# Kernel tuning notes

Hardware: AMD Instinct MI355X
Metric: run time of the kernel (lower is better)

The kernel has to match this reference:

```python
import jax, jax.numpy as jnp
import numpy as np

NUM_FEATURES = 256
NUM_PIDS = 5532
CQ_SIZE = 5000
N_NONID = 256
N = 2048
OIM_SCALAR = 30.0
MOMENTUM = 0.5


def _unit_rows(key, shape):
    v = jax.random.normal(key, shape, dtype=jnp.float32)
    return v / jnp.linalg.norm(v, axis=-1, keepdims=True)


def setup_inputs() -> dict:
    key = jax.random.key(0)
    ks = jax.random.split(key, 8)
    inputs = _unit_rows(ks[0], (N, NUM_FEATURES))
    targets = jax.random.randint(ks[1], (N,), 0, NUM_PIDS + 100, dtype=jnp.int32)
    belong_to_first_half = jax.random.randint(ks[2], (N,), 0, 2) > 0
    non_id_feat = _unit_rows(ks[3], (N_NONID, NUM_FEATURES))
    lut = _unit_rows(ks[4], (NUM_PIDS, NUM_FEATURES))
    cq = _unit_rows(ks[5], (CQ_SIZE, NUM_FEATURES))
    first_pos_sample = _unit_rows(ks[6], (NUM_PIDS, NUM_FEATURES))
    second_pos_sample = _unit_rows(ks[7], (NUM_PIDS, NUM_FEATURES))
    return {
        "inputs": inputs,
        "non_id_feat": non_id_feat,
        "lut": lut,
        "cq": cq,
        "first_pos_sample": first_pos_sample,
        "second_pos_sample": second_pos_sample,
        "targets": targets,
        "belong_to_first_half": belong_to_first_half,
        "header": 0,
    }


def reference(inputs, non_id_feat, lut, cq, first_pos_sample, second_pos_sample,
              targets, belong_to_first_half, header):
    # OIM forward: similarities against labeled LUT and [circular queue; non-id feats]
    out_labeled = inputs @ lut.T                                  # [N, num_pids]
    out_unlabeled = inputs @ jnp.concatenate([cq, non_id_feat], 0).T  # [N, cq+nonid]
    projected = jnp.concatenate([out_labeled, out_unlabeled], axis=1)
    return projected * OIM_SCALAR
```

## Files before the change

### kernel.cpp

```cpp
#include <hip/hip_runtime.h>
#include <hip/hip_bf16.h>
#include <stdint.h>
#include <stddef.h>

#define NUM_FEATURES 256
#define NUM_PIDS 5532
#define CQ_SIZE 5000
#define N_NONID 256
#define N_ROWS 2048
#define N_COLS (NUM_PIDS + CQ_SIZE + N_NONID)
#define OIM_SCALAR 30.0f


#define BM 128
#define BN 128
#define BK 64
#define KITERS (NUM_FEATURES / BK)

#define NT_PER_XCD 11
#define N_TILES 85
#define M_TILES 16
#define GRID_BLOCKS (8 * NT_PER_XCD * M_TILES)

#define B_ROWS_PAD (N_TILES * BN)
#define A_RB (N_ROWS / 16)
#define B_RB (B_ROWS_PAD / 16)
#define A_CHUNKS (A_RB * 8)
#define B_CHUNKS (B_RB * 8)
#define WS_A_BYTES ((size_t)A_CHUNKS * 1024)
#define WS_B_BYTES ((size_t)B_CHUNKS * 1024)
#define CONV_BLOCKS (((A_CHUNKS + B_CHUNKS) * 64) / 256)

typedef __bf16 bf16_t;
typedef __bf16 bf16x4 __attribute__((ext_vector_type(4)));
typedef __bf16 bf16x8 __attribute__((ext_vector_type(8)));
typedef float f32x4 __attribute__((ext_vector_type(4)));

__device__ __forceinline__ void gload16(const void* g, void* l) {
    __builtin_amdgcn_global_load_lds(
        (const __attribute__((address_space(1))) void*)g,
        (__attribute__((address_space(3))) void*)l, 16, 0, 0);
}

__global__ __launch_bounds__(256)
void oim_convert_kernel(const float* __restrict__ A, const float* __restrict__ lut,
                        const float* __restrict__ cq, const float* __restrict__ nonid,
                        bf16_t* __restrict__ Aperm, bf16_t* __restrict__ Bperm) {
    const int tid  = blockIdx.x * 256 + threadIdx.x;
    const int lane = tid & 63;
    const int g    = tid >> 6;
    const int lr   = lane & 15;
    const int khi  = (lane >> 4) * 8;

    const float* src = nullptr;
    bf16_t* dst;
    if (g < A_CHUNKS) {
        const int kc = g & 1, kt = (g >> 1) & 3, rb = g >> 3;
        const int row = rb * 16 + lr;
        const int k0  = kt * 64 + kc * 32 + khi;
        src = A + (size_t)row * NUM_FEATURES + k0;
        dst = Aperm + (size_t)g * 512 + lane * 8;
    } else {
        const int gb = g - A_CHUNKS;
        const int kc = gb & 1, kt = (gb >> 1) & 3, rb = gb >> 3;
        const int row = rb * 16 + lr;
        const int k0  = kt * 64 + kc * 32 + khi;
        dst = Bperm + (size_t)gb * 512 + lane * 8;
        if (row < NUM_PIDS)
            src = lut + (size_t)row * NUM_FEATURES + k0;
        else if (row < NUM_PIDS + CQ_SIZE)
            src = cq + (size_t)(row - NUM_PIDS) * NUM_FEATURES + k0;
        else if (row < N_COLS)
            src = nonid + (size_t)(row - NUM_PIDS - CQ_SIZE) * NUM_FEATURES + k0;
    }
    bf16x8 v = {(bf16_t)0.f, (bf16_t)0.f, (bf16_t)0.f, (bf16_t)0.f,
                (bf16_t)0.f, (bf16_t)0.f, (bf16_t)0.f, (bf16_t)0.f};
    if (src) {
        const float4 a = *(const float4*)src;
        const float4 b = *(const float4*)(src + 4);
        v = bf16x8{(bf16_t)a.x, (bf16_t)a.y, (bf16_t)a.z, (bf16_t)a.w,
                   (bf16_t)b.x, (bf16_t)b.y, (bf16_t)b.z, (bf16_t)b.w};
    }
    *(bf16x8*)dst = v;
}

__global__ __launch_bounds__(256)
void oim_gemm_dma(const bf16_t* __restrict__ Aperm, const bf16_t* __restrict__ Bperm,
                  float* __restrict__ out) {
    __shared__ __align__(16) bf16_t As[2][BM * BK];
    __shared__ __align__(16) bf16_t Bs[2][BN * BK];

    const int id  = blockIdx.x;
    const int xcd = id & 7;
    const int l   = id >> 3;
    const int nt  = xcd * NT_PER_XCD + l % NT_PER_XCD;
    const int mt  = l / NT_PER_XCD;
    if (nt >= N_TILES) return;
    const int m0 = mt * BM;
    const int n0 = nt * BN;

    const int tid  = threadIdx.x;
    const int wid  = tid >> 6;
    const int lane = tid & 63;

    const bf16_t* agp[4];
    const bf16_t* bgp[4];
    int ldsoff[4];
    #pragma unroll
    for (int j = 0; j < 4; ++j) {
        const int rbl = wid * 2 + (j >> 1);
        const int kc  = j & 1;
        agp[j] = Aperm + (size_t)(mt * 8 + rbl) * 4096 + kc * 512 + lane * 8;
        bgp[j] = Bperm + (size_t)(nt * 8 + rbl) * 4096 + kc * 512 + lane * 8;
        ldsoff[j] = (wid * 4 + j) * 512;
    }

    const int rbA0 = (wid >> 1) * 4;
    const int rbB0 = (wid & 1) * 4;

    f32x4 acc[4][4] = {};

    #pragma unroll
    for (int j = 0; j < 4; ++j) {
        gload16(agp[j], &As[0][ldsoff[j]]);
        gload16(bgp[j], &Bs[0][ldsoff[j]]);
    }
    __syncthreads();

    #pragma unroll
    for (int kt = 0; kt < KITERS; ++kt) {
        const bf16_t* const as = As[kt & 1];
        const bf16_t* const bs = Bs[kt & 1];
        if (kt < KITERS - 1) {
            bf16_t* const asn = As[(kt + 1) & 1];
            bf16_t* const bsn = Bs[(kt + 1) & 1];
            const int ko = (kt + 1) * 1024;
            #pragma unroll
            for (int j = 0; j < 4; ++j) {
                gload16(agp[j] + ko, &asn[ldsoff[j]]);
                gload16(bgp[j] + ko, &bsn[ldsoff[j]]);
            }
        }
        bf16x8 af[2][4], bfr[2][4];
        #pragma unroll
        for (int kc = 0; kc < 2; ++kc) {
            #pragma unroll
            for (int t = 0; t < 4; ++t) {
                af[kc][t]  = *(const bf16x8*)&as[(((rbA0 + t) * 2 + kc) * 64 + lane) * 8];
                bfr[kc][t] = *(const bf16x8*)&bs[(((rbB0 + t) * 2 + kc) * 64 + lane) * 8];
            }
        }
        #pragma unroll
        for (int kc = 0; kc < 2; ++kc)
            #pragma unroll
            for (int tm = 0; tm < 4; ++tm)
                #pragma unroll
                for (int tn = 0; tn < 4; ++tn)
                    acc[tm][tn] = __builtin_amdgcn_mfma_f32_16x16x32_bf16(
                        af[kc][tm], bfr[kc][tn], acc[tm][tn], 0, 0, 0);
        if (kt < KITERS - 1) __syncthreads();
    }

    const int wave_m = (wid >> 1) * 64;
    const int wave_n = (wid & 1) * 64;
    #pragma unroll
    for (int tm = 0; tm < 4; ++tm) {
        const int row_base = m0 + wave_m + tm * 16 + (lane >> 4) * 4;
        #pragma unroll
        for (int tn = 0; tn < 4; ++tn) {
            const int col = n0 + wave_n + tn * 16 + (lane & 15);
            if (col < N_COLS) {
                #pragma unroll
                for (int i = 0; i < 4; ++i)
                    out[(size_t)(row_base + i) * N_COLS + col] =
                        acc[tm][tn][i] * OIM_SCALAR;
            }
        }
    }
}

__global__ __launch_bounds__(256)
void oim_gemm_kernel(const float* __restrict__ A, const float* __restrict__ lut,
                     const float* __restrict__ cq, const float* __restrict__ nonid,
                     float* __restrict__ out) {
    __shared__ __align__(16) bf16_t As[2][BM * 32];
    __shared__ __align__(16) bf16_t Bs[2][BM * 32];

    const int id  = blockIdx.x;
    const int xcd = id & 7;
    const int l   = id >> 3;
    const int nt  = xcd * NT_PER_XCD + l % NT_PER_XCD;
    const int mt  = l / NT_PER_XCD;
    if (nt >= N_TILES) return;
    const int m0 = mt * BM;
    const int n0 = nt * BN;

    const int tid  = threadIdx.x;
    const int wid  = tid >> 6;
    const int lane = tid & 63;

    const int srow = tid >> 3;
    const int skk  = (tid & 7) * 4;

    const float* arow[4];
    const float* brow[4];
    #pragma unroll
    for (int j = 0; j < 4; ++j) {
        const int rm = m0 + srow + j * 32;
        arow[j] = A + (size_t)rm * NUM_FEATURES + skk;
        int r = n0 + srow + j * 32;
        r = r < (N_COLS - 1) ? r : (N_COLS - 1);
        const float* src;
        if (r < NUM_PIDS)                 src = lut   + (size_t)r * NUM_FEATURES;
        else if (r < NUM_PIDS + CQ_SIZE)  src = cq    + (size_t)(r - NUM_PIDS) * NUM_FEATURES;
        else                              src = nonid + (size_t)(r - NUM_PIDS - CQ_SIZE) * NUM_FEATURES;
        brow[j] = src + skk;
    }

    const int wave_m = (wid >> 1) * 64;
    const int wave_n = (wid & 1) * 64;
    const int fr = lane & 15;
    const int fk = (lane >> 4) * 8;

    f32x4 acc[4][4] = {};

    float4 areg[4], breg[4];
    #pragma unroll
    for (int j = 0; j < 4; ++j) {
        areg[j] = *(const float4*)arow[j];
        breg[j] = *(const float4*)brow[j];
        arow[j] += 32;
        brow[j] += 32;
    }

    #pragma unroll
    for (int kt = 0; kt < 8; ++kt) {
        bf16_t* const as = As[kt & 1];
        bf16_t* const bs = Bs[kt & 1];
        #pragma unroll
        for (int j = 0; j < 4; ++j) {
            const int ldix = (srow + j * 32) * 32 + skk;
            bf16x4 ac = { (bf16_t)areg[j].x, (bf16_t)areg[j].y,
                          (bf16_t)areg[j].z, (bf16_t)areg[j].w };
            bf16x4 bc = { (bf16_t)breg[j].x, (bf16_t)breg[j].y,
                          (bf16_t)breg[j].z, (bf16_t)breg[j].w };
            *(bf16x4*)&as[ldix] = ac;
            *(bf16x4*)&bs[ldix] = bc;
        }
        if (kt < 7) {
            #pragma unroll
            for (int j = 0; j < 4; ++j) {
                areg[j] = *(const float4*)arow[j];
                breg[j] = *(const float4*)brow[j];
                arow[j] += 32;
                brow[j] += 32;
            }
        }
        __syncthreads();

        bf16x8 af[4], bfr[4];
        #pragma unroll
        for (int t = 0; t < 4; ++t) {
            af[t]  = *(const bf16x8*)&as[(wave_m + t * 16 + fr) * 32 + fk];
            bfr[t] = *(const bf16x8*)&bs[(wave_n + t * 16 + fr) * 32 + fk];
        }
        #pragma unroll
        for (int tm = 0; tm < 4; ++tm)
            #pragma unroll
            for (int tn = 0; tn < 4; ++tn)
                acc[tm][tn] = __builtin_amdgcn_mfma_f32_16x16x32_bf16(
                    af[tm], bfr[tn], acc[tm][tn], 0, 0, 0);
    }

    #pragma unroll
    for (int tm = 0; tm < 4; ++tm) {
        const int row_base = m0 + wave_m + tm * 16 + (lane >> 4) * 4;
        #pragma unroll
        for (int tn = 0; tn < 4; ++tn) {
            const int col = n0 + wave_n + tn * 16 + (lane & 15);
            if (col < N_COLS) {
                #pragma unroll
                for (int i = 0; i < 4; ++i)
                    out[(size_t)(row_base + i) * N_COLS + col] =
                        acc[tm][tn][i] * OIM_SCALAR;
            }
        }
    }
}

extern "C" void kernel_launch(void* const* d_in, const int* in_sizes, int n_in,
                              void* d_out, int out_size, void* d_ws, size_t ws_size,
                              hipStream_t stream) {
    const float* inputs = (const float*)d_in[0];
    const float* nonid  = (const float*)d_in[1];
    const float* lut    = (const float*)d_in[2];
    const float* cq     = (const float*)d_in[3];
    float* out = (float*)d_out;

    const size_t ws_need = WS_A_BYTES + WS_B_BYTES;
    if (d_ws != nullptr && ws_size >= ws_need) {
        bf16_t* Aperm = (bf16_t*)d_ws;
        bf16_t* Bperm = (bf16_t*)((char*)d_ws + WS_A_BYTES);
        oim_convert_kernel<<<dim3(CONV_BLOCKS), 256, 0, stream>>>(
            inputs, lut, cq, nonid, Aperm, Bperm);
        oim_gemm_dma<<<dim3(GRID_BLOCKS), 256, 0, stream>>>(Aperm, Bperm, out);
    } else {
        oim_gemm_kernel<<<dim3(GRID_BLOCKS), 256, 0, stream>>>(
            inputs, lut, cq, nonid, out);
    }
}
```

Before: 137.5 us.

## Replace LDS-staged GEMM with direct global-to-register fragment loads

Drops the shared-memory double buffer, the global_load_lds DMA and the barriers from the GEMM. Each wave now loads its MFMA fragments straight from the pre-permuted bf16 workspace into registers, prefetching one K-slice ahead. The convert kernel's permutation is reordered so that each row block's eight K-slices are contiguous. Waves sharing a tile now each fetch the same A/B fragments from global memory, so the kernel leans on L2/L1 for reuse instead of LDS, which removes synchronisation but may add memory traffic.

```diff
diff --git a/kernel.cpp b/kernel.cpp
--- a/kernel.cpp
+++ b/kernel.cpp
@@ -14,8 +14,7 @@
 
 #define BM 128
 #define BN 128
-#define BK 64
-#define KITERS (NUM_FEATURES / BK)
+#define KITERS 4
 
 #define NT_PER_XCD 11
 #define N_TILES 85
@@ -35,12 +34,6 @@
 typedef __bf16 bf16x4 __attribute__((ext_vector_type(4)));
 typedef __bf16 bf16x8 __attribute__((ext_vector_type(8)));
 typedef float f32x4 __attribute__((ext_vector_type(4)));
-
-__device__ __forceinline__ void gload16(const void* g, void* l) {
-    __builtin_amdgcn_global_load_lds(
-        (const __attribute__((address_space(1))) void*)g,
-        (__attribute__((address_space(3))) void*)l, 16, 0, 0);
-}
 
 __global__ __launch_bounds__(256)
 void oim_convert_kernel(const float* __restrict__ A, const float* __restrict__ lut,
@@ -55,16 +48,16 @@
     const float* src = nullptr;
     bf16_t* dst;
     if (g < A_CHUNKS) {
-        const int kc = g & 1, kt = (g >> 1) & 3, rb = g >> 3;
+        const int ks = g & 7, rb = g >> 3;
         const int row = rb * 16 + lr;
-        const int k0  = kt * 64 + kc * 32 + khi;
+        const int k0  = ks * 32 + khi;
         src = A + (size_t)row * NUM_FEATURES + k0;
         dst = Aperm + (size_t)g * 512 + lane * 8;
     } else {
         const int gb = g - A_CHUNKS;
-        const int kc = gb & 1, kt = (gb >> 1) & 3, rb = gb >> 3;
+        const int ks = gb & 7, rb = gb >> 3;
         const int row = rb * 16 + lr;
-        const int k0  = kt * 64 + kc * 32 + khi;
+        const int k0  = ks * 32 + khi;
         dst = Bperm + (size_t)gb * 512 + lane * 8;
         if (row < NUM_PIDS)
             src = lut + (size_t)row * NUM_FEATURES + k0;
@@ -85,11 +78,8 @@
 }
 
 __global__ __launch_bounds__(256)
-void oim_gemm_dma(const bf16_t* __restrict__ Aperm, const bf16_t* __restrict__ Bperm,
+void oim_gemm_reg(const bf16_t* __restrict__ Aperm, const bf16_t* __restrict__ Bperm,
                   float* __restrict__ out) {
-    __shared__ __align__(16) bf16_t As[2][BM * BK];
-    __shared__ __align__(16) bf16_t Bs[2][BN * BK];
-
     const int id  = blockIdx.x;
     const int xcd = id & 7;
     const int l   = id >> 3;
@@ -103,62 +93,37 @@
     const int wid  = tid >> 6;
     const int lane = tid & 63;
 
-    const bf16_t* agp[4];
-    const bf16_t* bgp[4];
-    int ldsoff[4];
-    #pragma unroll
-    for (int j = 0; j < 4; ++j) {
-        const int rbl = wid * 2 + (j >> 1);
-        const int kc  = j & 1;
-        agp[j] = Aperm + (size_t)(mt * 8 + rbl) * 4096 + kc * 512 + lane * 8;
-        bgp[j] = Bperm + (size_t)(nt * 8 + rbl) * 4096 + kc * 512 + lane * 8;
-        ldsoff[j] = (wid * 4 + j) * 512;
-    }
-
     const int rbA0 = (wid >> 1) * 4;
     const int rbB0 = (wid & 1) * 4;
 
+    const bf16_t* abase = Aperm + ((size_t)(mt * 8 + rbA0) * 8) * 512 + lane * 8;
+    const bf16_t* bbase = Bperm + ((size_t)(nt * 8 + rbB0) * 8) * 512 + lane * 8;
+
     f32x4 acc[4][4] = {};
-
-    #pragma unroll
-    for (int j = 0; j < 4; ++j) {
-        gload16(agp[j], &As[0][ldsoff[j]]);
-        gload16(bgp[j], &Bs[0][ldsoff[j]]);
-    }
-    __syncthreads();
-
-    #pragma unroll
-    for (int kt = 0; kt < KITERS; ++kt) {
-        const bf16_t* const as = As[kt & 1];
-        const bf16_t* const bs = Bs[kt & 1];
-        if (kt < KITERS - 1) {
-            bf16_t* const asn = As[(kt + 1) & 1];
-            bf16_t* const bsn = Bs[(kt + 1) & 1];
-            const int ko = (kt + 1) * 1024;
-            #pragma unroll
-            for (int j = 0; j < 4; ++j) {
-                gload16(agp[j] + ko, &asn[ldsoff[j]]);
-                gload16(bgp[j] + ko, &bsn[ldsoff[j]]);
-            }
-        }
-        bf16x8 af[2][4], bfr[2][4];
-        #pragma unroll
-        for (int kc = 0; kc < 2; ++kc) {
+    bf16x8 af[2][4], bfr[2][4];
+
+    #pragma unroll
+    for (int t = 0; t < 4; ++t) {
+        af[0][t]  = *(const bf16x8*)(abase + (size_t)(t * 8 + 0) * 512);
+        bfr[0][t] = *(const bf16x8*)(bbase + (size_t)(t * 8 + 0) * 512);
+    }
+
+    #pragma unroll
+    for (int ks = 0; ks < 8; ++ks) {
+        const int cur = ks & 1, nxt = cur ^ 1;
+        if (ks < 7) {
             #pragma unroll
             for (int t = 0; t < 4; ++t) {
-                af[kc][t]  = *(const bf16x8*)&as[(((rbA0 + t) * 2 + kc) * 64 + lane) * 8];
-                bfr[kc][t] = *(const bf16x8*)&bs[(((rbB0 + t) * 2 + kc) * 64 + lane) * 8];
-            }
-        }
-        #pragma unroll
-        for (int kc = 0; kc < 2; ++kc)
-            #pragma unroll
-            for (int tm = 0; tm < 4; ++tm)
-                #pragma unroll
-                for (int tn = 0; tn < 4; ++tn)
-                    acc[tm][tn] = __builtin_amdgcn_mfma_f32_16x16x32_bf16(
-                        af[kc][tm], bfr[kc][tn], acc[tm][tn], 0, 0, 0);
-        if (kt < KITERS - 1) __syncthreads();
+                af[nxt][t]  = *(const bf16x8*)(abase + (size_t)(t * 8 + ks + 1) * 512);
+                bfr[nxt][t] = *(const bf16x8*)(bbase + (size_t)(t * 8 + ks + 1) * 512);
+            }
+        }
+        #pragma unroll
+        for (int tm = 0; tm < 4; ++tm)
+            #pragma unroll
+            for (int tn = 0; tn < 4; ++tn)
+                acc[tm][tn] = __builtin_amdgcn_mfma_f32_16x16x32_bf16(
+                    af[cur][tm], bfr[cur][tn], acc[tm][tn], 0, 0, 0);
     }
 
     const int wave_m = (wid >> 1) * 64;
@@ -303,7 +268,7 @@
         bf16_t* Bperm = (bf16_t*)((char*)d_ws + WS_A_BYTES);
         oim_convert_kernel<<<dim3(CONV_BLOCKS), 256, 0, stream>>>(
             inputs, lut, cq, nonid, Aperm, Bperm);
-        oim_gemm_dma<<<dim3(GRID_BLOCKS), 256, 0, stream>>>(Aperm, Bperm, out);
+        oim_gemm_reg<<<dim3(GRID_BLOCKS), 256, 0, stream>>>(Aperm, Bperm, out);
     } else {
         oim_gemm_kernel<<<dim3(GRID_BLOCKS), 256, 0, stream>>>(
             inputs, lut, cq, nonid, out);
```

Result: no change. 139.8 us (+1.7%).
